# Performance work log

Measured on AMD Instinct MI355X. Metric: run time of the kernel, lower is better.

Reference implementation:

```python
import jax, jax.numpy as jnp
import numpy as np

H = 32        # hiddenSize
OUT = 256     # output_size
T = 60        # num_frames
EPS = 1e-5


def setup_inputs() -> dict:
    key = jax.random.key(0)
    ks = jax.random.split(key, 16)
    s = 0.05
    rn = lambda k, shp: (jax.random.normal(k, shp, dtype=jnp.float32) * s)
    return {
        "x": jax.random.normal(ks[0], (1, T, 63), dtype=jnp.float32),
        "w00": rn(ks[1], (63, 63)), "b00": rn(ks[2], (63,)),
        "w01": rn(ks[3], (64, 63)), "b01": rn(ks[4], (64,)),
        "ln_g": jnp.ones((64,), jnp.float32), "ln_b": jnp.zeros((64,), jnp.float32),
        "w_ih": rn(ks[5], (4 * H, 64)), "w_hh": rn(ks[6], (4 * H, H)),
        "b_ih": rn(ks[7], (4 * H,)), "b_hh": rn(ks[8], (4 * H,)),
        "bn_g": jnp.ones((H,), jnp.float32), "bn_b": jnp.zeros((H,), jnp.float32),
        "w10": rn(ks[9], (32, H)), "b10": rn(ks[10], (32,)),
        "w11": rn(ks[11], (32, 32)), "b11": rn(ks[12], (32,)),
        "w12": rn(ks[13], (OUT, 32)), "b12": rn(ks[14], (OUT,)),
    }


def _forward(x, w00, b00, w01, b01, ln_g, ln_b, w_ih, w_hh, b_ih, b_hh,
             bn_g, bn_b, w10, b10, w11, b11, w12, b12):
    # x: [1, T, 63] -> scan over T frames (fused MLP + LayerNorm + LSTM cell)
    xs = jnp.transpose(x, (1, 0, 2))  # [T, 1, 63]

    def step(carry, xt):  # xt: [1, 63]
        h, c = carry
        f = jax.nn.relu(xt @ w00.T + b00)          # [1, 63]
        f = jax.nn.relu(f @ w01.T + b01)           # [1, 64]
        mu = jnp.mean(f, axis=-1, keepdims=True)
        var = jnp.mean((f - mu) ** 2, axis=-1, keepdims=True)
        f = (f - mu) * jax.lax.rsqrt(var + EPS) * ln_g + ln_b
        gates = f @ w_ih.T + b_ih + h @ w_hh.T + b_hh  # [1, 4H]
        i_g, f_g, g_g, o_g = jnp.split(gates, 4, axis=-1)
        c = jax.nn.sigmoid(f_g) * c + jax.nn.sigmoid(i_g) * jnp.tanh(g_g)
        h = jax.nn.sigmoid(o_g) * jnp.tanh(c)
        return (h, c), None

    h0 = jnp.zeros((1, H), x.dtype)
    c0 = jnp.zeros((1, H), x.dtype)
    (h, _), _ = jax.lax.scan(step, (h0, c0), xs)
    # BatchNorm1d in eval mode (running_mean=0, running_var=1)
    out = h * jax.lax.rsqrt(jnp.float32(1.0) + EPS) * bn_g + bn_b
    out = jax.nn.relu(out @ w10.T + b10)
    out = jax.nn.relu(out @ w11.T + b11)
    return out @ w12.T + b12  # [1, OUT]


def reference(x, w00, b00, w01, b01, ln_g, ln_b, w_ih, w_hh, b_ih, b_hh,
              bn_g, bn_b, w10, b10, w11, b11, w12, b12):
    return _forward(x, w00, b00, w01, b01, ln_g, ln_b, w_ih, w_hh, b_ih, b_hh,
                    bn_g, bn_b, w10, b10, w11, b11, w12, b12)
```

## Files before the change

kernel.cpp:

```cpp
#include <hip/hip_runtime.h>

#define EPS 1e-5f
#define MAGIC 0x5CA9F1A6u

typedef float v2f __attribute__((ext_vector_type(2)));

__device__ __forceinline__ float frcp(float x) { return __builtin_amdgcn_rcpf(x); }
__device__ __forceinline__ float fsigm(float x) { return frcp(1.0f + __expf(-x)); }
__device__ __forceinline__ float ftanh(float x) {
    float e = __expf(-2.0f * x);
    return (1.0f - e) * frcp(1.0f + e);
}
__device__ __forceinline__ float rdl32(float v, int k) {
    return __int_as_float(__builtin_amdgcn_readlane(__float_as_int(v), 32 + k));
}
__device__ __forceinline__ float xhalf_sum(float x) {
#if __has_builtin(__builtin_amdgcn_permlane32_swap)
    auto r = __builtin_amdgcn_permlane32_swap(__float_as_uint(x),
                                              __float_as_uint(x), false, false);
    return __uint_as_float(r[0]) + __uint_as_float(r[1]);
#else
    return x + __shfl_xor(x, 32);
#endif
}

__global__ __launch_bounds__(64) void fused_kernel(
    const float* __restrict__ x,
    const float* __restrict__ w00, const float* __restrict__ b00,
    const float* __restrict__ w01, const float* __restrict__ b01,
    const float* __restrict__ ln_g, const float* __restrict__ ln_b,
    const float* __restrict__ w_ih, const float* __restrict__ w_hh,
    const float* __restrict__ b_ih, const float* __restrict__ b_hh,
    const float* __restrict__ bn_g, const float* __restrict__ bn_b,
    const float* __restrict__ w10, const float* __restrict__ b10,
    const float* __restrict__ w11, const float* __restrict__ b11,
    const float* __restrict__ w12, const float* __restrict__ b12,
    float* __restrict__ Gx, unsigned* __restrict__ flags,
    float* __restrict__ out)
{
    __shared__ float smem[16324];
    const int j = threadIdx.x;

    if (blockIdx.x < 60) {
        const int t = blockIdx.x;
        float* w00s = smem;
        float* w01s = smem + 3972;
        float* wihT = smem + 8004;
        float* scr  = smem + 16196;

        {
            const float4* g4 = (const float4*)w00;
            float4* s4 = (float4*)w00s;
            for (int i = j; i < 992; i += 64) s4[i] = g4[i];
            if (j == 0) w00s[3968] = w00[3968];
        }
        {
            const float4* g4 = (const float4*)w01;
            float4* s4 = (float4*)w01s;
            for (int i = j; i < 1008; i += 64) s4[i] = g4[i];
        }
        for (int r = j; r < 128; r += 64) {
            const float4* row = (const float4*)(w_ih + r * 64);
            #pragma unroll
            for (int q = 0; q < 16; q++) {
                float4 v = row[q];
                wihT[(4 * q + 0) * 128 + r] = v.x;
                wihT[(4 * q + 1) * 128 + r] = v.y;
                wihT[(4 * q + 2) * 128 + r] = v.z;
                wihT[(4 * q + 3) * 128 + r] = v.w;
            }
        }
        scr[j] = (j < 63) ? x[t * 63 + j] : 0.0f;
        __syncthreads();

        float f0 = 0.0f;
        if (j < 63) {
            float acc = b00[j];
            const float* wr = w00s + j * 63;
            #pragma unroll
            for (int k = 0; k < 63; k++) acc += scr[k] * wr[k];
            f0 = fmaxf(acc, 0.0f);
        }
        __syncthreads();
        scr[j] = f0;
        __syncthreads();

        float acc = b01[j];
        {
            const float* wr = w01s + j * 63;
            #pragma unroll
            for (int k = 0; k < 63; k++) acc += scr[k] * wr[k];
        }
        float f1 = fmaxf(acc, 0.0f);

        float s = f1, sq = f1 * f1;
        #pragma unroll
        for (int off = 32; off > 0; off >>= 1) {
            s  += __shfl_xor(s, off);
            sq += __shfl_xor(sq, off);
        }
        float mu  = s * (1.0f / 64.0f);
        float var = sq * (1.0f / 64.0f) - mu * mu;
        float f   = (f1 - mu) * rsqrtf(var + EPS) * ln_g[j] + ln_b[j];
        __syncthreads();
        scr[64 + j] = f;
        __syncthreads();

        float a0 = b_ih[j] + b_hh[j];
        float a1 = b_ih[j + 64] + b_hh[j + 64];
        #pragma unroll
        for (int k = 0; k < 64; k++) {
            float fk = scr[64 + k];
            a0 += fk * wihT[k * 128 + j];
            a1 += fk * wihT[k * 128 + 64 + j];
        }
        Gx[t * 128 + j]      = a0;
        Gx[t * 128 + 64 + j] = a1;

        __threadfence();
        __syncthreads();
        if (j == 0)
            __hip_atomic_store(&flags[t], MAGIC, __ATOMIC_RELEASE,
                               __HIP_MEMORY_SCOPE_AGENT);
        return;
    }

    float* gxs = smem;

    v2f wAB[32];
    {
        const float4* r0 = (const float4*)(w_hh + j * 32);
        const float4* r1 = (const float4*)(w_hh + (j + 64) * 32);
        #pragma unroll
        for (int q = 0; q < 8; q++) {
            float4 a = r0[q];
            float4 b = r1[q];
            wAB[4 * q + 0] = (v2f){a.x, b.x};
            wAB[4 * q + 1] = (v2f){a.y, b.y};
            wAB[4 * q + 2] = (v2f){a.z, b.z};
            wAB[4 * q + 3] = (v2f){a.w, b.w};
        }
    }

    {
        bool done = (j >= 60);
        while (true) {
            if (!done)
                done = (__hip_atomic_load(&flags[j], __ATOMIC_RELAXED,
                                          __HIP_MEMORY_SCOPE_AGENT) == MAGIC);
            if (__ballot(done) == ~0ULL) break;
            __builtin_amdgcn_s_sleep(1);
        }
        (void)__hip_atomic_load(&flags[0], __ATOMIC_ACQUIRE,
                                __HIP_MEMORY_SCOPE_AGENT);
    }

    {
        const float4* g4 = (const float4*)Gx;
        float4* s4 = (float4*)gxs;
        for (int i = j; i < 1920; i += 64) s4[i] = g4[i];
        gxs[7680 + j] = 0.0f;
        gxs[7744 + j] = 0.0f;
    }
    __syncthreads();

    const bool low = (j < 32);
    float c = 0.0f, hn = 0.0f;
    float gA = gxs[j], gB = gxs[64 + j];
    for (int t = 0; t < 60; t++) {
        float hk[32];
        #pragma unroll
        for (int k = 0; k < 32; k++) hk[k] = rdl32(hn, k);

        v2f acc0 = {gA, gB};
        v2f acc1 = {0.f, 0.f};
        v2f acc2 = {0.f, 0.f};
        v2f acc3 = {0.f, 0.f};
        gA = gxs[(t + 1) * 128 + j];
        gB = gxs[(t + 1) * 128 + 64 + j];
        #pragma unroll
        for (int d = 0; d < 8; d++) {
            int k = d * 4;
            v2f h0 = {hk[k + 0], hk[k + 0]};
            v2f h1 = {hk[k + 1], hk[k + 1]};
            v2f h2 = {hk[k + 2], hk[k + 2]};
            v2f h3 = {hk[k + 3], hk[k + 3]};
            acc0 += h0 * wAB[k + 0];
            acc1 += h1 * wAB[k + 1];
            acc2 += h2 * wAB[k + 2];
            acc3 += h3 * wAB[k + 3];
        }
        v2f asum = (acc0 + acc1) + (acc2 + acc3);
        float a0 = asum.x;
        float a1 = asum.y;

        float e1 = __expf(-a1);
        float sO = frcp(1.0f + e1);
        float e2 = e1 * e1;
        float t1 = (1.0f - e2) * frcp(1.0f + e2);
        float s0 = fsigm(a0);
        float own = s0 * (low ? t1 : c);
        c = xhalf_sum(own);
        hn = sO * ftanh(c);
    }

    const float rs = rsqrtf(1.0f + EPS);
    const int ro = j & 31;
    float acc = b10[ro];
    #pragma unroll
    for (int k = 0; k < 32; k++) {
        float hkk = rdl32(hn, k);
        float hb = hkk * rs * bn_g[k] + bn_b[k];
        acc += w10[ro * 32 + k] * hb;
    }
    float o1 = fmaxf(acc, 0.0f);

    acc = b11[ro];
    #pragma unroll
    for (int k = 0; k < 32; k++)
        acc += w11[ro * 32 + k]
             * __int_as_float(__builtin_amdgcn_readlane(__float_as_int(o1), k));
    float o2 = fmaxf(acc, 0.0f);

    float a[4];
    #pragma unroll
    for (int r = 0; r < 4; r++) a[r] = b12[j + 64 * r];
    #pragma unroll
    for (int k = 0; k < 32; k++) {
        float h2 = __int_as_float(__builtin_amdgcn_readlane(__float_as_int(o2), k));
        #pragma unroll
        for (int r = 0; r < 4; r++) a[r] += w12[(j + 64 * r) * 32 + k] * h2;
    }
    #pragma unroll
    for (int r = 0; r < 4; r++) out[j + 64 * r] = a[r];
}

extern "C" void kernel_launch(void* const* d_in, const int* in_sizes, int n_in,
                              void* d_out, int out_size, void* d_ws, size_t ws_size,
                              hipStream_t stream) {
    const float* x    = (const float*)d_in[0];
    const float* w00  = (const float*)d_in[1];
    const float* b00  = (const float*)d_in[2];
    const float* w01  = (const float*)d_in[3];
    const float* b01  = (const float*)d_in[4];
    const float* ln_g = (const float*)d_in[5];
    const float* ln_b = (const float*)d_in[6];
    const float* w_ih = (const float*)d_in[7];
    const float* w_hh = (const float*)d_in[8];
    const float* b_ih = (const float*)d_in[9];
    const float* b_hh = (const float*)d_in[10];
    const float* bn_g = (const float*)d_in[11];
    const float* bn_b = (const float*)d_in[12];
    const float* w10  = (const float*)d_in[13];
    const float* b10  = (const float*)d_in[14];
    const float* w11  = (const float*)d_in[15];
    const float* b11  = (const float*)d_in[16];
    const float* w12  = (const float*)d_in[17];
    const float* b12  = (const float*)d_in[18];
    float* out = (float*)d_out;
    float*    Gx    = (float*)d_ws;
    unsigned* flags = (unsigned*)((char*)d_ws + 49152);

    fused_kernel<<<61, 64, 0, stream>>>(x, w00, b00, w01, b01, ln_g, ln_b,
                                        w_ih, w_hh, b_ih, b_hh, bn_g, bn_b,
                                        w10, b10, w11, b11, w12, b12,
                                        Gx, flags, out);
}
```

Measured before the change: 124.5 us.

## Compute all four LSTM gates per lane, removing cross-half exchange

Each lane now holds all four gate weight rows (i, f, g, o) for one hidden unit, so the whole cell update happens within a lane. Before, the gates were split across the two 32-lane halves and combined with a permlane swap. This removes the cross-half exchange and the select from the serial per-step dependency chain. In exchange each lane does twice the recurrent FMAs and holds twice the weight registers, and the upper 32 lanes duplicate the work of the lower 32.

Result: slower. 130.1 us (+4.5%).

```diff
diff --git a/kernel.cpp b/kernel.cpp
--- a/kernel.cpp
+++ b/kernel.cpp
@@ -11,17 +11,8 @@
     float e = __expf(-2.0f * x);
     return (1.0f - e) * frcp(1.0f + e);
 }
-__device__ __forceinline__ float rdl32(float v, int k) {
-    return __int_as_float(__builtin_amdgcn_readlane(__float_as_int(v), 32 + k));
-}
-__device__ __forceinline__ float xhalf_sum(float x) {
-#if __has_builtin(__builtin_amdgcn_permlane32_swap)
-    auto r = __builtin_amdgcn_permlane32_swap(__float_as_uint(x),
-                                              __float_as_uint(x), false, false);
-    return __uint_as_float(r[0]) + __uint_as_float(r[1]);
-#else
-    return x + __shfl_xor(x, 32);
-#endif
+__device__ __forceinline__ float rdl(float v, int k) {
+    return __int_as_float(__builtin_amdgcn_readlane(__float_as_int(v), k));
 }
 
 __global__ __launch_bounds__(64) void fused_kernel(
@@ -126,19 +117,21 @@
     }
 
     float* gxs = smem;
-
-    v2f wAB[32];
+    const int m = j & 31;
+
+    v2f wIF[32], wGO[32];
     {
-        const float4* r0 = (const float4*)(w_hh + j * 32);
-        const float4* r1 = (const float4*)(w_hh + (j + 64) * 32);
+        const float4* ri = (const float4*)(w_hh + (     m) * 32);
+        const float4* rf = (const float4*)(w_hh + (32 + m) * 32);
+        const float4* rg = (const float4*)(w_hh + (64 + m) * 32);
+        const float4* ro = (const float4*)(w_hh + (96 + m) * 32);
         #pragma unroll
         for (int q = 0; q < 8; q++) {
-            float4 a = r0[q];
-            float4 b = r1[q];
-            wAB[4 * q + 0] = (v2f){a.x, b.x};
-            wAB[4 * q + 1] = (v2f){a.y, b.y};
-            wAB[4 * q + 2] = (v2f){a.z, b.z};
-            wAB[4 * q + 3] = (v2f){a.w, b.w};
+            float4 vi = ri[q], vf = rf[q], vg = rg[q], vo = ro[q];
+            wIF[4 * q + 0] = (v2f){vi.x, vf.x};  wGO[4 * q + 0] = (v2f){vg.x, vo.x};
+            wIF[4 * q + 1] = (v2f){vi.y, vf.y};  wGO[4 * q + 1] = (v2f){vg.y, vo.y};
+            wIF[4 * q + 2] = (v2f){vi.z, vf.z};  wGO[4 * q + 2] = (v2f){vg.z, vo.z};
+            wIF[4 * q + 3] = (v2f){vi.w, vf.w};  wGO[4 * q + 3] = (v2f){vg.w, vo.w};
         }
     }
 
@@ -164,20 +157,19 @@
     }
     __syncthreads();
 
-    const bool low = (j < 32);
     float c = 0.0f, hn = 0.0f;
-    float gA = gxs[j], gB = gxs[64 + j];
+    float gi = gxs[m], gf = gxs[32 + m], gg = gxs[64 + m], go = gxs[96 + m];
     for (int t = 0; t < 60; t++) {
         float hk[32];
         #pragma unroll
-        for (int k = 0; k < 32; k++) hk[k] = rdl32(hn, k);
-
-        v2f acc0 = {gA, gB};
-        v2f acc1 = {0.f, 0.f};
-        v2f acc2 = {0.f, 0.f};
-        v2f acc3 = {0.f, 0.f};
-        gA = gxs[(t + 1) * 128 + j];
-        gB = gxs[(t + 1) * 128 + 64 + j];
+        for (int k = 0; k < 32; k++) hk[k] = rdl(hn, k);
+
+        v2f aIF0 = {gi, gf}, aIF1 = {0.f, 0.f}, aIF2 = {0.f, 0.f}, aIF3 = {0.f, 0.f};
+        v2f aGO0 = {gg, go}, aGO1 = {0.f, 0.f}, aGO2 = {0.f, 0.f}, aGO3 = {0.f, 0.f};
+        gi = gxs[(t + 1) * 128 +      m];
+        gf = gxs[(t + 1) * 128 + 32 + m];
+        gg = gxs[(t + 1) * 128 + 64 + m];
+        go = gxs[(t + 1) * 128 + 96 + m];
         #pragma unroll
         for (int d = 0; d < 8; d++) {
             int k = d * 4;
@@ -185,23 +177,20 @@
             v2f h1 = {hk[k + 1], hk[k + 1]};
             v2f h2 = {hk[k + 2], hk[k + 2]};
             v2f h3 = {hk[k + 3], hk[k + 3]};
-            acc0 += h0 * wAB[k + 0];
-            acc1 += h1 * wAB[k + 1];
-            acc2 += h2 * wAB[k + 2];
-            acc3 += h3 * wAB[k + 3];
-        }
-        v2f asum = (acc0 + acc1) + (acc2 + acc3);
-        float a0 = asum.x;
-        float a1 = asum.y;
-
-        float e1 = __expf(-a1);
-        float sO = frcp(1.0f + e1);
-        float e2 = e1 * e1;
-        float t1 = (1.0f - e2) * frcp(1.0f + e2);
-        float s0 = fsigm(a0);
-        float own = s0 * (low ? t1 : c);
-        c = xhalf_sum(own);
-        hn = sO * ftanh(c);
+            aIF0 += h0 * wIF[k + 0];  aGO0 += h0 * wGO[k + 0];
+            aIF1 += h1 * wIF[k + 1];  aGO1 += h1 * wGO[k + 1];
+            aIF2 += h2 * wIF[k + 2];  aGO2 += h2 * wGO[k + 2];
+            aIF3 += h3 * wIF[k + 3];  aGO3 += h3 * wGO[k + 3];
+        }
+        v2f aIF = (aIF0 + aIF1) + (aIF2 + aIF3);
+        v2f aGO = (aGO0 + aGO1) + (aGO2 + aGO3);
+
+        float si = fsigm(aIF.x);
+        float sf = fsigm(aIF.y);
+        float tg = ftanh(aGO.x);
+        float so = fsigm(aGO.y);
+        c  = sf * c + si * tg;
+        hn = so * ftanh(c);
     }
 
     const float rs = rsqrtf(1.0f + EPS);
@@ -209,7 +198,7 @@
     float acc = b10[ro];
     #pragma unroll
     for (int k = 0; k < 32; k++) {
-        float hkk = rdl32(hn, k);
+        float hkk = rdl(hn, k);
         float hb = hkk * rs * bn_g[k] + bn_b[k];
         acc += w10[ro * 32 + k] * hb;
     }
@@ -217,9 +206,7 @@
 
     acc = b11[ro];
     #pragma unroll
-    for (int k = 0; k < 32; k++)
-        acc += w11[ro * 32 + k]
-             * __int_as_float(__builtin_amdgcn_readlane(__float_as_int(o1), k));
+    for (int k = 0; k < 32; k++) acc += w11[ro * 32 + k] * rdl(o1, k);
     float o2 = fmaxf(acc, 0.0f);
 
     float a[4];
@@ -227,7 +214,7 @@
     for (int r = 0; r < 4; r++) a[r] = b12[j + 64 * r];
     #pragma unroll
     for (int k = 0; k < 32; k++) {
-        float h2 = __int_as_float(__builtin_amdgcn_readlane(__float_as_int(o2), k));
+        float h2 = rdl(o2, k);
         #pragma unroll
         for (int r = 0; r < 4; r++) a[r] += w12[(j + 64 * r) * 32 + k] * h2;
     }
```
